# Kernel tuning notes

Measured on AMD Instinct MI355X. Metric: run time of the kernel, lower is better.

Reference implementation:

```python
import jax, jax.numpy as jnp
import numpy as np

DIM = 320
D_STATE = 32
D_CONV = 4
EXPAND = 2
HEADDIM = 80
D_INNER = EXPAND * DIM          # 640
NHEADS = D_INNER // HEADDIM     # 8
NGROUPS = 1
CONV_DIM = D_INNER + 2 * NGROUPS * D_STATE          # 704
D_IN_PROJ = 2 * D_INNER + 2 * NGROUPS * D_STATE + NHEADS  # 1352
PATCH = (16, 16, 16)
NUM_PT_EMB = 2


def setup_inputs() -> dict:
    key = jax.random.key(0)
    ks = jax.random.split(key, 16)
    B, Np = 4, 8
    x = jax.random.normal(ks[0], (B, DIM) + PATCH, dtype=jnp.float32)
    point_coords = jax.random.uniform(ks[1], (B, Np, 3), dtype=jnp.float32) * jnp.asarray(PATCH, jnp.float32)
    point_labels = jax.random.randint(ks[2], (B, Np), 0, 2)
    return {
        "x": x,
        "point_coords": point_coords,
        "ln_w": jnp.ones((DIM,), jnp.float32),
        "ln_b": jnp.zeros((DIM,), jnp.float32),
        "in_proj_w": jax.random.normal(ks[3], (D_IN_PROJ, DIM), jnp.float32) * 0.02,
        "conv_w": jax.random.normal(ks[4], (CONV_DIM, 1, D_CONV), jnp.float32) * 0.2,
        "conv_b": jax.random.normal(ks[5], (CONV_DIM,), jnp.float32) * 0.02,
        "dt_bias": jax.random.uniform(ks[6], (NHEADS,), jnp.float32, 0.0, 0.1),
        "A_log": jnp.log(jax.random.uniform(ks[7], (NHEADS,), jnp.float32, 1.0, 16.0)),
        "Dp": jnp.ones((NHEADS,), jnp.float32),
        "rms_w": jnp.ones((D_INNER,), jnp.float32),
        "out_proj_w": jax.random.normal(ks[8], (DIM, D_INNER), jnp.float32) * 0.02,
        "pe_gauss": jax.random.normal(ks[9], (3, DIM // 2), jnp.float32),
        "point_embed": jax.random.normal(ks[10], (NUM_PT_EMB, DIM), jnp.float32) * 0.02,
        "not_a_point": jax.random.normal(ks[11], (DIM,), jnp.float32) * 0.02,
        "point_labels": point_labels,
    }


def _forward(x, point_coords, ln_w, ln_b, in_proj_w, conv_w, conv_b, dt_bias,
             A_log, Dp, rms_w, out_proj_w, pe_gauss, point_embed, not_a_point,
             point_labels):
    B, C = x.shape[:2]
    img_dims = x.shape[2:]
    n_tokens = int(np.prod(img_dims))
    xf = x.reshape(B, C, n_tokens).transpose(0, 2, 1)  # (B, T, C)

    # ---- PointEncoder (SAM-style random Fourier positional embedding) ----
    pc = point_coords / jnp.asarray(PATCH, x.dtype)     # normalize to [0,1]
    pc = 2.0 * pc - 1.0
    pe = (2.0 * jnp.pi) * (pc @ pe_gauss)               # (B, Np, DIM/2)
    pemb = jnp.concatenate([jnp.sin(pe), jnp.cos(pe)], axis=-1)  # (B, Np, DIM)
    lbl = point_labels[..., None]
    safe = jnp.clip(point_labels, 0, NUM_PT_EMB - 1)
    pemb = jnp.where(lbl == -1, not_a_point, pemb + point_embed[safe])

    seq = jnp.concatenate([xf, pemb], axis=1)           # (B, L, C)
    L = seq.shape[1]

    # ---- LayerNorm ----
    mu = seq.mean(-1, keepdims=True)
    var = jnp.mean((seq - mu) ** 2, axis=-1, keepdims=True)
    xn = (seq - mu) * jax.lax.rsqrt(var + 1e-5) * ln_w + ln_b

    # ---- Mamba2 ----
    zxbcdt = xn @ in_proj_w.T                            # (B, L, 1352)
    z = zxbcdt[..., :D_INNER]
    xBC = zxbcdt[..., D_INNER:D_INNER + CONV_DIM]
    dt = zxbcdt[..., D_INNER + CONV_DIM:]                # (B, L, H)
    dt = jax.nn.softplus(dt + dt_bias)

    # causal depthwise conv1d over channels
    conv = jax.lax.conv_general_dilated(
        xBC.transpose(0, 2, 1), conv_w, (1,), [(D_CONV - 1, 0)],
        feature_group_count=CONV_DIM,
        dimension_numbers=("NCH", "OIH", "NCH"))
    xBC = jax.nn.silu((conv + conv_b[None, :, None]).transpose(0, 2, 1))

    xs = xBC[..., :D_INNER].reshape(B, L, NHEADS, HEADDIM)
    Bm = xBC[..., D_INNER:D_INNER + D_STATE]             # (B, L, N), ngroups=1
    Cm = xBC[..., D_INNER + D_STATE:]                    # (B, L, N)

    A = -jnp.exp(A_log)                                  # (H,)
    dA = jnp.exp(dt * A)                                 # (B, L, H)

    def step(h, inp):
        dA_t, dt_t, B_t, C_t, x_t = inp
        h = h * dA_t[:, :, None, None] + jnp.einsum('bh,bn,bhp->bhpn', dt_t, B_t, x_t)
        y = jnp.einsum('bhpn,bn->bhp', h, C_t)
        return h, y

    inps = (dA.transpose(1, 0, 2), dt.transpose(1, 0, 2),
            Bm.transpose(1, 0, 2), Cm.transpose(1, 0, 2),
            xs.transpose(1, 0, 2, 3))
    h0 = jnp.zeros((B, NHEADS, HEADDIM, D_STATE), x.dtype)
    _, ys = jax.lax.scan(step, h0, inps)                 # (L, B, H, P)
    y = ys.transpose(1, 0, 2, 3) + xs * Dp[None, None, :, None]
    y = y.reshape(B, L, D_INNER)

    # gated RMSNorm
    y = y * jax.nn.silu(z)
    y = y * jax.lax.rsqrt(jnp.mean(y * y, axis=-1, keepdims=True) + 1e-5) * rms_w
    out = y @ out_proj_w.T                               # (B, L, DIM)

    out = out[:, :n_tokens].transpose(0, 2, 1).reshape(B, C, *img_dims)
    return out


def reference(x, point_coords, ln_w, ln_b, in_proj_w, conv_w, conv_b, dt_bias,
              A_log, Dp, rms_w, out_proj_w, pe_gauss, point_embed, not_a_point,
              point_labels):
    return _forward(x, point_coords, ln_w, ln_b, in_proj_w, conv_w, conv_b,
                    dt_bias, A_log, Dp, rms_w, out_proj_w, pe_gauss,
                    point_embed, not_a_point, point_labels)
```

## Files before the change

### kernel.cpp

```cpp
#include <hip/hip_runtime.h>
#include <math.h>

#define BQ 4
#define LQ 4104
#define NTQ 4096
#define CDIM 320
#define DIP 1352
#define DI 640
#define CONVD 704
#define NH 8
#define HD 80
#define DS 32
#define MQ (BQ*LQ)
#define QC 64
#define NC 65

typedef __attribute__((ext_vector_type(8))) short bf16x8;
typedef __attribute__((ext_vector_type(4))) float f32x4;

__device__ __forceinline__ unsigned short f2bf(float f){
  union { float f; unsigned u; } v; v.f = f;
  unsigned r = v.u + 0x7FFFu + ((v.u >> 16) & 1u);
  return (unsigned short)(r >> 16);
}
__device__ __forceinline__ float bf2f(unsigned short u){
  union { unsigned u; float f; } v; v.u = ((unsigned)u) << 16;
  return v.f;
}
__device__ __forceinline__ float warp_sum(float v){
  #pragma unroll
  for (int o = 32; o; o >>= 1) v += __shfl_xor(v, o);
  return v;
}
__device__ __forceinline__ void gload16(const unsigned short* g, unsigned short* l){
  __builtin_amdgcn_global_load_lds(
      (const __attribute__((address_space(1))) unsigned int*)g,
      (__attribute__((address_space(3))) unsigned int*)l, 16, 0, 0);
}
__device__ __forceinline__ int swz64(int p, int i){
  return p*QC + (i ^ ((p & 7) << 3));
}

__global__ __launch_bounds__(256) void k_f2bf4(
    const float* __restrict__ s1, unsigned short* __restrict__ d1, int n14,
    const float* __restrict__ s2, unsigned short* __restrict__ d2, int n24)
{
  int i4 = blockIdx.x*256 + threadIdx.x;
  if (i4 < n14) {
    float4 v = ((const float4*)s1)[i4];
    unsigned short o[4] = {f2bf(v.x), f2bf(v.y), f2bf(v.z), f2bf(v.w)};
    *(uint2*)&d1[i4*4] = *(const uint2*)o;
  } else if (i4 - n14 < n24) {
    int j = i4 - n14;
    float4 v = ((const float4*)s2)[j];
    unsigned short o[4] = {f2bf(v.x), f2bf(v.y), f2bf(v.z), f2bf(v.w)};
    *(uint2*)&d2[j*4] = *(const uint2*)o;
  }
}

__global__ __launch_bounds__(256) void k_stats(
    const float* __restrict__ x, float* __restrict__ muP, float* __restrict__ s2P)
{
  int b = blockIdx.z;
  int sl = blockIdx.y;
  int cs0 = sl * 40;
  int tok = blockIdx.x*256 + threadIdx.x;
  const float* xb = x + ((size_t)b*CDIM)*NTQ;
  float s = 0.f, s2 = 0.f;
  #pragma unroll 8
  for (int c = cs0; c < cs0 + 40; c++) {
    float v = xb[(size_t)c*NTQ + tok];
    s += v; s2 = fmaf(v, v, s2);
  }
  muP[((size_t)sl*BQ + b)*NTQ + tok] = s;
  s2P[((size_t)sl*BQ + b)*NTQ + tok] = s2;
}

__global__ __launch_bounds__(256) void k_norm_t(
    const float* __restrict__ x, const float* __restrict__ muP,
    const float* __restrict__ s2P, const float* __restrict__ lnw,
    const float* __restrict__ lnb, unsigned short* __restrict__ xnh)
{
  int b = blockIdx.z;
  int c0 = blockIdx.y * 64;
  int t0 = blockIdx.x * 64;
  int t = threadIdx.x;
  int lt = t & 63, cg = t >> 6;
  const float* xb = x + ((size_t)b*CDIM)*NTQ;

  __shared__ unsigned short T[64][72];
  __shared__ float muL[64], rsL[64];
  if (t < 64) {
    float s = 0.f, s2 = 0.f;
    #pragma unroll
    for (int sl = 0; sl < 8; sl++) {
      s  += muP[((size_t)sl*BQ + b)*NTQ + t0 + t];
      s2 += s2P[((size_t)sl*BQ + b)*NTQ + t0 + t];
    }
    float mu = s*(1.0f/CDIM);
    muL[t] = mu;
    rsL[t] = rsqrtf(s2*(1.0f/CDIM) - mu*mu + 1e-5f);
  }
  __syncthreads();
  float mu = muL[lt], rs = rsL[lt];
  #pragma unroll
  for (int c = cg; c < 64; c += 4) {
    float v = xb[(size_t)(c0+c)*NTQ + t0 + lt];
    T[lt][c] = f2bf((v - mu)*rs*lnw[c0+c] + lnb[c0+c]);
  }
  __syncthreads();
  #pragma unroll
  for (int i = 0; i < 4; i++) {
    int idx = t + 256*i;
    int tok = idx >> 4, cq = idx & 15;
    *(uint2*)&xnh[((size_t)(b*LQ) + t0 + tok)*CDIM + c0 + cq*4] =
        *(const uint2*)&T[tok][cq*4];
  }
}

__global__ __launch_bounds__(320) void k_pt_ln(
    const float* __restrict__ pcoords, const float* __restrict__ lnw,
    const float* __restrict__ lnb, const float* __restrict__ pgauss,
    const float* __restrict__ pemb_w, const float* __restrict__ nap,
    const int* __restrict__ plabels, unsigned short* __restrict__ xnh)
{
  int j = blockIdx.x, b = blockIdx.y;
  int c = threadIdx.x;
  int f = (c < 160) ? c : c - 160;
  float p0 = pcoords[(b*8+j)*3+0]*(2.0f/16.0f) - 1.0f;
  float p1 = pcoords[(b*8+j)*3+1]*(2.0f/16.0f) - 1.0f;
  float p2 = pcoords[(b*8+j)*3+2]*(2.0f/16.0f) - 1.0f;
  float pe = 6.283185307179586f*(p0*pgauss[f] + p1*pgauss[160+f] + p2*pgauss[320+f]);
  float pv = (c < 160) ? sinf(pe) : cosf(pe);
  int lab = plabels[b*8+j];
  float val;
  if (lab == -1) val = nap[c];
  else {
    int safe = lab < 0 ? 0 : (lab > 1 ? 1 : lab);
    val = pv + pemb_w[safe*CDIM + c];
  }
  float s  = warp_sum(val);
  float s2 = warp_sum(val*val);
  __shared__ float r1[5], r2[5];
  int w = threadIdx.x >> 6, lane = threadIdx.x & 63;
  if (lane == 0) { r1[w] = s; r2[w] = s2; }
  __syncthreads();
  float ts = 0.f, ts2 = 0.f;
  #pragma unroll
  for (int i = 0; i < 5; i++) { ts += r1[i]; ts2 += r2[i]; }
  float mu  = ts * (1.0f/CDIM);
  float var = ts2 * (1.0f/CDIM) - mu*mu;
  float rsig = rsqrtf(var + 1e-5f);
  xnh[((size_t)b*LQ + NTQ + j)*CDIM + c] = f2bf((val - mu)*rsig*lnw[c] + lnb[c]);
}

__global__ __launch_bounds__(256) void k_gemm1_mfma(
    const unsigned short* __restrict__ Abf, const unsigned short* __restrict__ Wbf,
    unsigned short* __restrict__ zxh, float* __restrict__ dtraw)
{
  __shared__ unsigned short As[2][128*32];
  __shared__ unsigned short Bs[2][128*32];
  int id = blockIdx.x;
  int xcd = id & 7, pos = id >> 3;
  const int q = 177, r = 3;
  int swz = (xcd < r ? xcd*(q+1) : r*(q+1) + (xcd-r)*q) + pos;
  int m0 = (swz / 11) * 128;
  int n0 = (swz % 11) * 128;
  int tid = threadIdx.x;
  int lane = tid & 63, wid = tid >> 6;
  int wr = wid >> 1, wc = wid & 1;
  int fr = lane & 15, fq = lane >> 4;
  int srow = lane >> 2;
  int scol = (lane & 3) * 8;

#define G1_STAGE(buf, kk)                                                   \
  {                                                                         \
    _Pragma("unroll")                                                       \
    for (int i = 0; i < 2; i++) {                                           \
      int seg = wid + i*4;                                                  \
      int rowA = seg*16 + srow;                                             \
      int ga = m0 + rowA; if (ga > MQ-1) ga = MQ-1;                         \
      gload16(Abf + (size_t)ga*CDIM + (kk) + scol, &As[buf][seg*512]);      \
      int gb = n0 + rowA; if (gb > DIP-1) gb = DIP-1;                       \
      gload16(Wbf + (size_t)gb*CDIM + (kk) + scol, &Bs[buf][seg*512]);      \
    }                                                                       \
  }

#define G1_COMPUTE(buf)                                                     \
  {                                                                         \
    bf16x8 fa[4], fb[4];                                                    \
    _Pragma("unroll")                                                       \
    for (int i = 0; i < 4; i++) {                                           \
      fa[i] = *(const bf16x8*)&As[buf][(wr*64 + i*16 + fr)*32 + fq*8];      \
      fb[i] = *(const bf16x8*)&Bs[buf][(wc*64 + i*16 + fr)*32 + fq*8];      \
    }                                                                       \
    _Pragma("unroll")                                                       \
    for (int i = 0; i < 4; i++)                                             \
      _Pragma("unroll")                                                     \
      for (int j = 0; j < 4; j++)                                           \
        acc[i][j] = __builtin_amdgcn_mfma_f32_16x16x32_bf16(fa[i], fb[j], acc[i][j], 0, 0, 0); \
  }

  f32x4 acc[4][4] = {};
  G1_STAGE(0, 0);
  __syncthreads();
  int cur = 0;
  for (int k0 = 32; k0 < CDIM; k0 += 32) {
    G1_STAGE(cur^1, k0);
    G1_COMPUTE(cur);
    __syncthreads();
    cur ^= 1;
  }
  G1_COMPUTE(cur);

  #pragma unroll
  for (int i = 0; i < 4; i++) {
    #pragma unroll
    for (int j = 0; j < 4; j++) {
      #pragma unroll
      for (int rr = 0; rr < 4; rr++) {
        int grow = m0 + wr*64 + i*16 + fq*4 + rr;
        int gcol = n0 + wc*64 + j*16 + fr;
        if (grow < MQ && gcol < DIP) {
          float v = acc[i][j][rr];
          zxh[(size_t)grow*DIP + gcol] = f2bf(v);
          if (gcol >= DI + CONVD)
            dtraw[(size_t)grow*NH + (gcol - (DI + CONVD))] = v;
        }
      }
    }
  }
}

__global__ __launch_bounds__(256) void k_conv(
    const unsigned short* __restrict__ zxh, const float* __restrict__ cw,
    const float* __restrict__ cb, unsigned short* __restrict__ xcb)
{
  const int nC4 = CONVD/4;
  int gid = blockIdx.x*256 + threadIdx.x;
  if (gid >= (MQ/8)*nC4) return;
  int c4 = gid % nC4;
  int mb = gid / nC4;
  int m0 = mb*8;
  int l0 = m0 % LQ;
  int c0 = c4*4;
  float4 cbv = *(const float4*)(cb + c0);
  float4 w0 = *(const float4*)(cw + (c0+0)*4);
  float4 w1 = *(const float4*)(cw + (c0+1)*4);
  float4 w2 = *(const float4*)(cw + (c0+2)*4);
  float4 w3 = *(const float4*)(cw + (c0+3)*4);
  const float* wp[4] = {(const float*)&w0, (const float*)&w1,
                        (const float*)&w2, (const float*)&w3};
  float vals[11][4];
  #pragma unroll
  for (int r = 0; r < 11; r++) {
    int ls = l0 - 3 + r;
    uint2 u = make_uint2(0,0);
    if (ls >= 0)
      u = *(const uint2*)(zxh + (size_t)(m0-3+r)*DIP + DI + c0);
    vals[r][0] = bf2f((unsigned short)(u.x & 0xffff));
    vals[r][1] = bf2f((unsigned short)(u.x >> 16));
    vals[r][2] = bf2f((unsigned short)(u.y & 0xffff));
    vals[r][3] = bf2f((unsigned short)(u.y >> 16));
  }
  const float* cbp = (const float*)&cbv;
  #pragma unroll
  for (int u = 0; u < 8; u++) {
    unsigned short o[4];
    #pragma unroll
    for (int ch = 0; ch < 4; ch++) {
      float a = cbp[ch];
      #pragma unroll
      for (int j = 0; j < 4; j++)
        a = fmaf(vals[u+j][ch], wp[ch][j], a);
      o[ch] = f2bf(a / (1.f + __expf(-a)));
    }
    *(uint2*)(xcb + (size_t)(m0+u)*CONVD + c0) = *(const uint2*)o;
  }
}

__global__ __launch_bounds__(256) void k_cumsum_state(
    const float* __restrict__ dtraw, const float* __restrict__ dt_bias,
    const float* __restrict__ A_log, const unsigned short* __restrict__ xcb,
    float* __restrict__ dtb, float* __restrict__ cs, float* __restrict__ Dc,
    float* __restrict__ Sbuf)
{
  int c = blockIdx.x, h = blockIdx.y, b = blockIdx.z;
  int len = LQ - c*QC; if (len > QC) len = QC;
  int t = threadIdx.x;
  int lane = t & 63, wid = t >> 6;
  int fr = lane & 15, fq = lane >> 4;
  int m0 = b*LQ + c*QC;

  __shared__ unsigned short XT[HD*QC];
  __shared__ unsigned short BwT[DS*QC];
  __shared__ float ws[QC];

  for (int idx = t; idx < (HD/8)*QC; idx += 256) {
    int pg = idx % 10, i = idx / 10;
    uint4 v = make_uint4(0,0,0,0);
    if (i < len)
      v = *(const uint4*)(xcb + (size_t)(m0+i)*CONVD + h*HD + pg*8);
    union { uint4 u; unsigned short us[8]; } cv; cv.u = v;
    #pragma unroll
    for (int e = 0; e < 8; e++)
      XT[swz64(pg*8+e, i)] = cv.us[e];
  }

  if (t < QC) {
    float A = -expf(A_log[h]);
    float sp = 0.f;
    if (t < len) {
      float v = dtraw[((size_t)(m0+t))*NH + h] + dt_bias[h];
      sp = (v > 20.f) ? v : log1pf(expf(v));
      dtb[((size_t)(m0+t))*NH + h] = sp;
    }
    float a = sp * A;
    #pragma unroll
    for (int off = 1; off < 64; off <<= 1) {
      float pv = __shfl_up(a, off, 64);
      if (t >= off) a += pv;
    }
    cs[((size_t)(b*NH+h)*NC + c)*QC + t] = a;
    if (t == len-1) Dc[(b*NH+h)*NC + c] = expf(a);
    float aEnd = __shfl(a, len-1, 64);
    ws[t] = (t < len) ? __expf(aEnd - a) * sp : 0.f;
  }
  __syncthreads();
  for (int idx = t; idx < DS*QC; idx += 256) {
    int n = idx & 31, i = idx >> 5;
    float v = (i < len) ? bf2f(xcb[(size_t)(m0+i)*CONVD + DI + n]) * ws[i] : 0.f;
    BwT[swz64(n, i)] = f2bf(v);
  }
  __syncthreads();

  size_t base = ((size_t)(b*NC + c)*NH + h)*(HD*DS);
  for (int tp = wid; tp < 10; tp += 4) {
    int pi = tp >> 1, ni = tp & 1;
    f32x4 acc = {};
    #pragma unroll
    for (int ks = 0; ks < 2; ks++) {
      bf16x8 fa = *(const bf16x8*)&XT[swz64(pi*16 + fr, ks*32 + fq*8)];
      bf16x8 fb = *(const bf16x8*)&BwT[swz64(ni*16 + fr, ks*32 + fq*8)];
      acc = __builtin_amdgcn_mfma_f32_16x16x32_bf16(fa, fb, acc, 0, 0, 0);
    }
    #pragma unroll
    for (int rr = 0; rr < 4; rr++)
      Sbuf[base + (size_t)(pi*16 + fq*4 + rr)*DS + ni*16 + fr] = acc[rr];
  }
}

__global__ __launch_bounds__(256) void k_state_scan(
    float* __restrict__ Sbuf, const float* __restrict__ Dc,
    float* __restrict__ H0)
{
  int tid = blockIdx.x*256 + threadIdx.x;
  int pn = tid % (HD*DS);
  int bh = tid / (HD*DS);
  int b = bh >> 3, h = bh & 7;
  float hst = 0.f;
  for (int c = 0; c < NC; c++) {
    size_t idx = ((size_t)(b*NC + c)*NH + h)*(HD*DS) + pn;
    float sv = Sbuf[idx];
    H0[idx] = hst;
    hst = hst * Dc[bh*NC + c] + sv;
  }
}

__global__ __launch_bounds__(256) void k_chunk_y_mfma(
    const unsigned short* __restrict__ xcb, const unsigned short* __restrict__ zxh,
    const float* __restrict__ dtb, const float* __restrict__ cs,
    const float* __restrict__ H0, const float* __restrict__ Dp,
    unsigned short* __restrict__ ygb)
{
  int c = blockIdx.x, h = blockIdx.y, b = blockIdx.z;
  int len = LQ - c*QC; if (len > QC) len = QC;
  int t = threadIdx.x;
  int lane = t & 63, wid = t >> 6;
  int fr = lane & 15, fq = lane >> 4;
  int m0 = b*LQ + c*QC;

  __shared__ unsigned short XT[HD*QC];
  __shared__ unsigned short Wt[4*16*32];
  __shared__ float slA[QC], dtlA[QC], elA[QC];

  const float* csb = cs + ((size_t)(b*NH+h)*NC + c)*QC;

  for (int idx = t; idx < (HD/8)*QC; idx += 256) {
    int pg = idx % 10, i = idx / 10;
    uint4 v = make_uint4(0,0,0,0);
    if (i < len)
      v = *(const uint4*)(xcb + (size_t)(m0+i)*CONVD + h*HD + pg*8);
    union { uint4 u; unsigned short us[8]; } cv; cv.u = v;
    #pragma unroll
    for (int e = 0; e < 8; e++)
      XT[swz64(pg*8+e, i)] = cv.us[e];
  }
  if (t < QC) {
    float s = csb[t];
    slA[t] = s;
    elA[t] = __expf(s);
    dtlA[t] = (t < len) ? dtb[((size_t)(m0+t))*NH + h] : 0.f;
  }
  __syncthreads();

  int row16 = wid*16 + fr;
  bf16x8 fa = {};
  if (row16 < len)
    fa = *(const bf16x8*)(xcb + (size_t)(m0+row16)*CONVD + DI + DS + fq*8);

  size_t hb = ((size_t)(b*NC + c)*NH + h)*(HD*DS);
  f32x4 acc[5];
  #pragma unroll
  for (int j = 0; j < 5; j++) {
    int p = j*16 + fr;
    const float* hp = H0 + hb + (size_t)p*DS + fq*8;
    float4 ha = *(const float4*)hp;
    float4 hbv = *(const float4*)(hp + 4);
    bf16x8 fb;
    fb[0]=(short)f2bf(ha.x);  fb[1]=(short)f2bf(ha.y);
    fb[2]=(short)f2bf(ha.z);  fb[3]=(short)f2bf(ha.w);
    fb[4]=(short)f2bf(hbv.x); fb[5]=(short)f2bf(hbv.y);
    fb[6]=(short)f2bf(hbv.z); fb[7]=(short)f2bf(hbv.w);
    f32x4 z = {};
    acc[j] = __builtin_amdgcn_mfma_f32_16x16x32_bf16(fa, fb, z, 0, 0, 0);
  }
  #pragma unroll
  for (int rr = 0; rr < 4; rr++) {
    float el = elA[wid*16 + fq*4 + rr];
    #pragma unroll
    for (int j = 0; j < 5; j++) acc[j][rr] *= el;
  }

  int wbase = wid << 9;
  for (int sc = 0; sc < 2; sc++) {
    int i0 = sc*32;
    #pragma unroll
    for (int jt = 0; jt < 2; jt++) {
      int col = i0 + jt*16 + fr;
      bf16x8 fbv = {};
      if (col < len)
        fbv = *(const bf16x8*)(xcb + (size_t)(m0+col)*CONVD + DI + fq*8);
      float sc_col = slA[col], dt_col = dtlA[col];
      f32x4 z = {};
      f32x4 g = __builtin_amdgcn_mfma_f32_16x16x32_bf16(fa, fbv, z, 0, 0, 0);
      #pragma unroll
      for (int rr = 0; rr < 4; rr++) {
        int lr = fq*4 + rr;
        int row = wid*16 + lr;
        float v = 0.f;
        if (col <= row)
          v = g[rr] * __expf(slA[row] - sc_col) * dt_col;
        int lc = jt*16 + fr;
        int slot = (lc >> 3) ^ (lr & 3);
        Wt[wbase + (lr<<5) + (slot<<3) + (lc&7)] = f2bf(v);
      }
    }
    bf16x8 wa = *(const bf16x8*)&Wt[wbase + (fr<<5) + ((fq ^ (fr&3))<<3)];
    #pragma unroll
    for (int j = 0; j < 5; j++) {
      int p = j*16 + fr;
      bf16x8 xb = *(const bf16x8*)&XT[swz64(p, i0 + fq*8)];
      acc[j] = __builtin_amdgcn_mfma_f32_16x16x32_bf16(wa, xb, acc[j], 0, 0, 0);
    }
  }

  float dpv = Dp[h];
  #pragma unroll
  for (int rr = 0; rr < 4; rr++) {
    int l = wid*16 + fq*4 + rr;
    if (l >= len) continue;
    size_t m = m0 + l;
    #pragma unroll
    for (int j = 0; j < 5; j++) {
      int p = j*16 + fr;
      int cc = h*HD + p;
      float xv = bf2f(XT[swz64(p, l)]);
      float y = acc[j][rr] + xv*dpv;
      float zv = bf2f(zxh[m*DIP + cc]);
      y *= zv / (1.f + __expf(-zv));
      ygb[m*DI + cc] = f2bf(y);
    }
  }
}

__global__ __launch_bounds__(256) void k_rms_scale(
    unsigned short* __restrict__ ygb, const float* __restrict__ rsw)
{
  int t = threadIdx.x;
  int grp = t >> 5;
  int gl = t & 31;
  size_t m = (size_t)blockIdx.x*8 + grp;
  unsigned short* row = ygb + m*DI;
  float v[5][4];
  float ss = 0.f;
  #pragma unroll
  for (int k = 0; k < 5; k++) {
    uint2 u = *(const uint2*)(row + (gl + 32*k)*4);
    v[k][0] = bf2f((unsigned short)(u.x & 0xffff));
    v[k][1] = bf2f((unsigned short)(u.x >> 16));
    v[k][2] = bf2f((unsigned short)(u.y & 0xffff));
    v[k][3] = bf2f((unsigned short)(u.y >> 16));
    ss += v[k][0]*v[k][0] + v[k][1]*v[k][1] + v[k][2]*v[k][2] + v[k][3]*v[k][3];
  }
  #pragma unroll
  for (int o = 16; o; o >>= 1) ss += __shfl_xor(ss, o, 32);
  float rsv = rsqrtf(ss*(1.0f/DI) + 1e-5f);
  #pragma unroll
  for (int k = 0; k < 5; k++) {
    float4 wv = *(const float4*)(rsw + (gl + 32*k)*4);
    unsigned short o4[4];
    o4[0] = f2bf(v[k][0]*rsv*wv.x);
    o4[1] = f2bf(v[k][1]*rsv*wv.y);
    o4[2] = f2bf(v[k][2]*rsv*wv.z);
    o4[3] = f2bf(v[k][3]*rsv*wv.w);
    *(uint2*)(row + (gl + 32*k)*4) = *(const uint2*)o4;
  }
}

__global__ __launch_bounds__(256) void k_gemm2_mfma(
    const unsigned short* __restrict__ W2h, const unsigned short* __restrict__ Ygh,
    float* __restrict__ out)
{
  __shared__ unsigned short As[2][128*32];
  __shared__ unsigned short Bs[2][128*32];
  int id = blockIdx.x;
  int xcd = id & 7, pos = id >> 3;
  const int q = 48, r = 3;
  int swz = (xcd < r ? xcd*(q+1) : r*(q+1) + (xcd-r)*q) + pos;
  int c0 = (swz % 3) * 128;
  int t0 = (swz / 3) * 128;
  int tid = threadIdx.x;
  int lane = tid & 63, wid = tid >> 6;
  int wr = wid >> 1, wc = wid & 1;
  int fr = lane & 15, fq = lane >> 4;
  int srow = lane >> 2;
  int scol = (lane & 3) * 8;

#define G2_STAGE(buf, kk)                                                   \
  {                                                                         \
    _Pragma("unroll")                                                       \
    for (int i = 0; i < 2; i++) {                                           \
      int seg = wid + i*4;                                                  \
      int rowA = seg*16 + srow;                                             \
      int ga = c0 + rowA; if (ga > CDIM-1) ga = CDIM-1;                     \
      gload16(W2h + (size_t)ga*DI + (kk) + scol, &As[buf][seg*512]);        \
      int gb = t0 + rowA; if (gb > MQ-1) gb = MQ-1;                         \
      gload16(Ygh + (size_t)gb*DI + (kk) + scol, &Bs[buf][seg*512]);        \
    }                                                                       \
  }

#define G2_COMPUTE(buf)                                                     \
  {                                                                         \
    bf16x8 fa[4], fb[4];                                                    \
    _Pragma("unroll")                                                       \
    for (int i = 0; i < 4; i++) {                                           \
      fa[i] = *(const bf16x8*)&As[buf][(wr*64 + i*16 + fr)*32 + fq*8];      \
      fb[i] = *(const bf16x8*)&Bs[buf][(wc*64 + i*16 + fr)*32 + fq*8];      \
    }                                                                       \
    _Pragma("unroll")                                                       \
    for (int i = 0; i < 4; i++)                                             \
      _Pragma("unroll")                                                     \
      for (int j = 0; j < 4; j++)                                           \
        acc[i][j] = __builtin_amdgcn_mfma_f32_16x16x32_bf16(fa[i], fb[j], acc[i][j], 0, 0, 0); \
  }

  f32x4 acc[4][4] = {};
  G2_STAGE(0, 0);
  __syncthreads();
  int cur = 0;
  for (int k0 = 32; k0 < DI; k0 += 32) {
    G2_STAGE(cur^1, k0);
    G2_COMPUTE(cur);
    __syncthreads();
    cur ^= 1;
  }
  G2_COMPUTE(cur);

  #pragma unroll
  for (int i = 0; i < 4; i++) {
    #pragma unroll
    for (int j = 0; j < 4; j++) {
      #pragma unroll
      for (int rr = 0; rr < 4; rr++) {
        int ch  = c0 + wr*64 + i*16 + fq*4 + rr;
        int tok = t0 + wc*64 + j*16 + fr;
        if (ch < CDIM && tok < MQ) {
          int b = tok / LQ, l = tok % LQ;
          if (l < NTQ)
            out[((size_t)(b*CDIM + ch))*NTQ + l] = acc[i][j][rr];
        }
      }
    }
  }
}

extern "C" void kernel_launch(void* const* d_in, const int* in_sizes, int n_in,
                              void* d_out, int out_size, void* d_ws, size_t ws_size,
                              hipStream_t stream)
{
  const float* x       = (const float*)d_in[0];
  const float* pc      = (const float*)d_in[1];
  const float* lnw     = (const float*)d_in[2];
  const float* lnb     = (const float*)d_in[3];
  const float* w1      = (const float*)d_in[4];
  const float* cw      = (const float*)d_in[5];
  const float* cb      = (const float*)d_in[6];
  const float* dt_bias = (const float*)d_in[7];
  const float* A_log   = (const float*)d_in[8];
  const float* Dp      = (const float*)d_in[9];
  const float* rsw     = (const float*)d_in[10];
  const float* w2      = (const float*)d_in[11];
  const float* pg      = (const float*)d_in[12];
  const float* pew     = (const float*)d_in[13];
  const float* nap     = (const float*)d_in[14];
  const int*   plab    = (const int*)d_in[15];
  float* out = (float*)d_out;

  unsigned short* xnh  = (unsigned short*)d_ws;
  unsigned short* zxh  = xnh + (size_t)MQ*CDIM;
  float* dtraw = (float*)(zxh + (size_t)MQ*DIP);
  unsigned short* xcb  = (unsigned short*)(dtraw + (size_t)MQ*NH);
  float* dtb = (float*)(xcb + (size_t)MQ*CONVD);
  float* cs  = dtb + (size_t)MQ*NH;
  float* Dc  = cs  + (size_t)BQ*NH*NC*QC;
  float* Sb  = Dc  + (size_t)BQ*NH*NC;
  float* H0  = Sb;
  unsigned short* ygb = (unsigned short*)(Sb + (size_t)BQ*NC*NH*HD*DS);
  unsigned short* w1h = ygb + (size_t)MQ*DI;
  unsigned short* w2h = w1h + (size_t)DIP*CDIM;
  float* muP = (float*)(w2h + (size_t)CDIM*DI);
  float* s2P = muP + (size_t)8*BQ*NTQ;

  k_f2bf4<<<((DIP*CDIM + CDIM*DI)/4 + 255)/256, 256, 0, stream>>>(
      w1, w1h, DIP*CDIM/4, w2, w2h, CDIM*DI/4);
  dim3 gs(NTQ/256, 8, BQ);
  k_stats<<<gs, 256, 0, stream>>>(x, muP, s2P);
  dim3 gn(NTQ/64, CDIM/64, BQ);
  k_norm_t<<<gn, 256, 0, stream>>>(x, muP, s2P, lnw, lnb, xnh);
  dim3 gp(8, BQ);
  k_pt_ln<<<gp, 320, 0, stream>>>(pc, lnw, lnb, pg, pew, nap, plab, xnh);
  k_gemm1_mfma<<<129*11, 256, 0, stream>>>(xnh, w1h, zxh, dtraw);
  k_conv<<<((MQ/8)*(CONVD/4) + 255)/256, 256, 0, stream>>>(zxh, cw, cb, xcb);
  dim3 gc(NC, NH, BQ);
  k_cumsum_state<<<gc, 256, 0, stream>>>(dtraw, dt_bias, A_log, xcb, dtb, cs, Dc, Sb);
  k_state_scan<<<(BQ*NH*HD*DS)/256, 256, 0, stream>>>(Sb, Dc, H0);
  k_chunk_y_mfma<<<gc, 256, 0, stream>>>(xcb, zxh, dtb, cs, H0, Dp, ygb);
  k_rms_scale<<<MQ/8, 256, 0, stream>>>(ygb, rsw);
  k_gemm2_mfma<<<129*3, 256, 0, stream>>>(w2h, ygb, out);
}
```

Before: 159.4 us.

## Fold RMSNorm into out-proj epilogue, merge prep kernels, store chunk states as bf16

Removes the separate RMS-scale pass. The chunk-y kernel now emits per-head sum-of-squares partials, the rms weight is folded into the bf16 out-proj weights, and gemm2 applies the per-token rsqrt in its epilogue. The weight conversion, LayerNorm stats and point-embedding kernels are merged into one launch, and the state scan writes bf16 initial states so chunk-y loads them directly. This cuts launches and a full read-modify-write of the y buffer. In exchange it adds a small ssum8 buffer, and the RMS statistic is now taken from fp32 y before bf16 rounding.

```diff
diff --git a/kernel.cpp b/kernel.cpp
--- a/kernel.cpp
+++ b/kernel.cpp
@@ -41,39 +41,90 @@
   return p*QC + (i ^ ((p & 7) << 3));
 }
 
-__global__ __launch_bounds__(256) void k_f2bf4(
-    const float* __restrict__ s1, unsigned short* __restrict__ d1, int n14,
-    const float* __restrict__ s2, unsigned short* __restrict__ d2, int n24)
-{
-  int i4 = blockIdx.x*256 + threadIdx.x;
-  if (i4 < n14) {
-    float4 v = ((const float4*)s1)[i4];
-    unsigned short o[4] = {f2bf(v.x), f2bf(v.y), f2bf(v.z), f2bf(v.w)};
-    *(uint2*)&d1[i4*4] = *(const uint2*)o;
-  } else if (i4 - n14 < n24) {
-    int j = i4 - n14;
-    float4 v = ((const float4*)s2)[j];
-    unsigned short o[4] = {f2bf(v.x), f2bf(v.y), f2bf(v.z), f2bf(v.w)};
-    *(uint2*)&d2[j*4] = *(const uint2*)o;
-  }
-}
-
-__global__ __launch_bounds__(256) void k_stats(
-    const float* __restrict__ x, float* __restrict__ muP, float* __restrict__ s2P)
-{
-  int b = blockIdx.z;
-  int sl = blockIdx.y;
-  int cs0 = sl * 40;
-  int tok = blockIdx.x*256 + threadIdx.x;
-  const float* xb = x + ((size_t)b*CDIM)*NTQ;
-  float s = 0.f, s2 = 0.f;
-  #pragma unroll 8
-  for (int c = cs0; c < cs0 + 40; c++) {
-    float v = xb[(size_t)c*NTQ + tok];
-    s += v; s2 = fmaf(v, v, s2);
-  }
-  muP[((size_t)sl*BQ + b)*NTQ + tok] = s;
-  s2P[((size_t)sl*BQ + b)*NTQ + tok] = s2;
+__global__ __launch_bounds__(256) void k_prep(
+    const float* __restrict__ w1, unsigned short* __restrict__ w1h,
+    const float* __restrict__ w2, const float* __restrict__ rsw,
+    unsigned short* __restrict__ w2h,
+    const float* __restrict__ x, float* __restrict__ muP, float* __restrict__ s2P,
+    const float* __restrict__ pcoords, const float* __restrict__ lnw,
+    const float* __restrict__ lnb, const float* __restrict__ pgauss,
+    const float* __restrict__ pemb_w, const float* __restrict__ nap,
+    const int* __restrict__ plabels, unsigned short* __restrict__ xnh)
+{
+  const int N1 = DIP*CDIM/4;
+  const int N2 = CDIM*DI/4;
+  const int NBW = (N1 + N2 + 255)/256;
+  int bid = blockIdx.x;
+  int t = threadIdx.x;
+
+  if (bid < NBW) {
+    int i4 = bid*256 + t;
+    if (i4 < N1) {
+      float4 v = ((const float4*)w1)[i4];
+      unsigned short o[4] = {f2bf(v.x), f2bf(v.y), f2bf(v.z), f2bf(v.w)};
+      *(uint2*)&w1h[i4*4] = *(const uint2*)o;
+    } else if (i4 - N1 < N2) {
+      int j = i4 - N1;
+      float4 v = ((const float4*)w2)[j];
+      float4 wv = *(const float4*)(rsw + (j*4) % DI);
+      unsigned short o[4] = {f2bf(v.x*wv.x), f2bf(v.y*wv.y),
+                             f2bf(v.z*wv.z), f2bf(v.w*wv.w)};
+      *(uint2*)&w2h[j*4] = *(const uint2*)o;
+    }
+    return;
+  }
+  bid -= NBW;
+  if (bid < 512) {
+    int xblk = bid & 15, sl = (bid >> 4) & 7, b = bid >> 7;
+    int cs0 = sl * 40;
+    int tok = xblk*256 + t;
+    const float* xb = x + ((size_t)b*CDIM)*NTQ;
+    float s = 0.f, s2 = 0.f;
+    #pragma unroll 8
+    for (int c = cs0; c < cs0 + 40; c++) {
+      float v = xb[(size_t)c*NTQ + tok];
+      s += v; s2 = fmaf(v, v, s2);
+    }
+    muP[((size_t)sl*BQ + b)*NTQ + tok] = s;
+    s2P[((size_t)sl*BQ + b)*NTQ + tok] = s2;
+    return;
+  }
+  bid -= 512;
+  int j = bid & 7, b = bid >> 3;
+  float p0 = pcoords[(b*8+j)*3+0]*(2.0f/16.0f) - 1.0f;
+  float p1 = pcoords[(b*8+j)*3+1]*(2.0f/16.0f) - 1.0f;
+  float p2 = pcoords[(b*8+j)*3+2]*(2.0f/16.0f) - 1.0f;
+  int lab = plabels[b*8+j];
+  int safe = lab < 0 ? 0 : (lab > 1 ? 1 : lab);
+  float vA, vB = 0.f;
+  {
+    int cc = t;
+    int f = (cc < 160) ? cc : cc - 160;
+    float pe = 6.283185307179586f*(p0*pgauss[f] + p1*pgauss[160+f] + p2*pgauss[320+f]);
+    float pv = (cc < 160) ? sinf(pe) : cosf(pe);
+    vA = (lab == -1) ? nap[cc] : pv + pemb_w[safe*CDIM + cc];
+  }
+  if (t < 64) {
+    int cc = t + 256;
+    int f = cc - 160;
+    float pe = 6.283185307179586f*(p0*pgauss[f] + p1*pgauss[160+f] + p2*pgauss[320+f]);
+    float pv = cosf(pe);
+    vB = (lab == -1) ? nap[cc] : pv + pemb_w[safe*CDIM + cc];
+  }
+  float s  = warp_sum(vA + vB);
+  float s2 = warp_sum(vA*vA + vB*vB);
+  __shared__ float r1[4], r2[4];
+  int w = t >> 6, lane = t & 63;
+  if (lane == 0) { r1[w] = s; r2[w] = s2; }
+  __syncthreads();
+  float ts  = r1[0]+r1[1]+r1[2]+r1[3];
+  float ts2 = r2[0]+r2[1]+r2[2]+r2[3];
+  float mu   = ts * (1.0f/CDIM);
+  float rsig = rsqrtf(ts2*(1.0f/CDIM) - mu*mu + 1e-5f);
+  size_t base = ((size_t)b*LQ + NTQ + j)*CDIM;
+  xnh[base + t] = f2bf((vA - mu)*rsig*lnw[t] + lnb[t]);
+  if (t < 64)
+    xnh[base + t + 256] = f2bf((vB - mu)*rsig*lnw[t+256] + lnb[t+256]);
 }
 
 __global__ __launch_bounds__(256) void k_norm_t(
@@ -116,42 +167,6 @@
     *(uint2*)&xnh[((size_t)(b*LQ) + t0 + tok)*CDIM + c0 + cq*4] =
         *(const uint2*)&T[tok][cq*4];
   }
-}
-
-__global__ __launch_bounds__(320) void k_pt_ln(
-    const float* __restrict__ pcoords, const float* __restrict__ lnw,
-    const float* __restrict__ lnb, const float* __restrict__ pgauss,
-    const float* __restrict__ pemb_w, const float* __restrict__ nap,
-    const int* __restrict__ plabels, unsigned short* __restrict__ xnh)
-{
-  int j = blockIdx.x, b = blockIdx.y;
-  int c = threadIdx.x;
-  int f = (c < 160) ? c : c - 160;
-  float p0 = pcoords[(b*8+j)*3+0]*(2.0f/16.0f) - 1.0f;
-  float p1 = pcoords[(b*8+j)*3+1]*(2.0f/16.0f) - 1.0f;
-  float p2 = pcoords[(b*8+j)*3+2]*(2.0f/16.0f) - 1.0f;
-  float pe = 6.283185307179586f*(p0*pgauss[f] + p1*pgauss[160+f] + p2*pgauss[320+f]);
-  float pv = (c < 160) ? sinf(pe) : cosf(pe);
-  int lab = plabels[b*8+j];
-  float val;
-  if (lab == -1) val = nap[c];
-  else {
-    int safe = lab < 0 ? 0 : (lab > 1 ? 1 : lab);
-    val = pv + pemb_w[safe*CDIM + c];
-  }
-  float s  = warp_sum(val);
-  float s2 = warp_sum(val*val);
-  __shared__ float r1[5], r2[5];
-  int w = threadIdx.x >> 6, lane = threadIdx.x & 63;
-  if (lane == 0) { r1[w] = s; r2[w] = s2; }
-  __syncthreads();
-  float ts = 0.f, ts2 = 0.f;
-  #pragma unroll
-  for (int i = 0; i < 5; i++) { ts += r1[i]; ts2 += r2[i]; }
-  float mu  = ts * (1.0f/CDIM);
-  float var = ts2 * (1.0f/CDIM) - mu*mu;
-  float rsig = rsqrtf(var + 1e-5f);
-  xnh[((size_t)b*LQ + NTQ + j)*CDIM + c] = f2bf((val - mu)*rsig*lnw[c] + lnb[c]);
 }
 
 __global__ __launch_bounds__(256) void k_gemm1_mfma(
@@ -351,8 +366,8 @@
 }
 
 __global__ __launch_bounds__(256) void k_state_scan(
-    float* __restrict__ Sbuf, const float* __restrict__ Dc,
-    float* __restrict__ H0)
+    const float* __restrict__ Sbuf, const float* __restrict__ Dc,
+    unsigned short* __restrict__ H0h)
 {
   int tid = blockIdx.x*256 + threadIdx.x;
   int pn = tid % (HD*DS);
@@ -362,7 +377,7 @@
   for (int c = 0; c < NC; c++) {
     size_t idx = ((size_t)(b*NC + c)*NH + h)*(HD*DS) + pn;
     float sv = Sbuf[idx];
-    H0[idx] = hst;
+    H0h[idx] = f2bf(hst);
     hst = hst * Dc[bh*NC + c] + sv;
   }
 }
@@ -370,8 +385,8 @@
 __global__ __launch_bounds__(256) void k_chunk_y_mfma(
     const unsigned short* __restrict__ xcb, const unsigned short* __restrict__ zxh,
     const float* __restrict__ dtb, const float* __restrict__ cs,
-    const float* __restrict__ H0, const float* __restrict__ Dp,
-    unsigned short* __restrict__ ygb)
+    const unsigned short* __restrict__ H0h, const float* __restrict__ Dp,
+    unsigned short* __restrict__ ygb, float* __restrict__ ssum8)
 {
   int c = blockIdx.x, h = blockIdx.y, b = blockIdx.z;
   int len = LQ - c*QC; if (len > QC) len = QC;
@@ -414,14 +429,7 @@
   #pragma unroll
   for (int j = 0; j < 5; j++) {
     int p = j*16 + fr;
-    const float* hp = H0 + hb + (size_t)p*DS + fq*8;
-    float4 ha = *(const float4*)hp;
-    float4 hbv = *(const float4*)(hp + 4);
-    bf16x8 fb;
-    fb[0]=(short)f2bf(ha.x);  fb[1]=(short)f2bf(ha.y);
-    fb[2]=(short)f2bf(ha.z);  fb[3]=(short)f2bf(ha.w);
-    fb[4]=(short)f2bf(hbv.x); fb[5]=(short)f2bf(hbv.y);
-    fb[6]=(short)f2bf(hbv.z); fb[7]=(short)f2bf(hbv.w);
+    bf16x8 fb = *(const bf16x8*)(H0h + hb + (size_t)p*DS + fq*8);
     f32x4 z = {};
     acc[j] = __builtin_amdgcn_mfma_f32_16x16x32_bf16(fa, fb, z, 0, 0, 0);
   }
@@ -471,6 +479,7 @@
     int l = wid*16 + fq*4 + rr;
     if (l >= len) continue;
     size_t m = m0 + l;
+    float ssp = 0.f;
     #pragma unroll
     for (int j = 0; j < 5; j++) {
       int p = j*16 + fr;
@@ -480,47 +489,17 @@
       float zv = bf2f(zxh[m*DIP + cc]);
       y *= zv / (1.f + __expf(-zv));
       ygb[m*DI + cc] = f2bf(y);
-    }
-  }
-}
-
-__global__ __launch_bounds__(256) void k_rms_scale(
-    unsigned short* __restrict__ ygb, const float* __restrict__ rsw)
-{
-  int t = threadIdx.x;
-  int grp = t >> 5;
-  int gl = t & 31;
-  size_t m = (size_t)blockIdx.x*8 + grp;
-  unsigned short* row = ygb + m*DI;
-  float v[5][4];
-  float ss = 0.f;
-  #pragma unroll
-  for (int k = 0; k < 5; k++) {
-    uint2 u = *(const uint2*)(row + (gl + 32*k)*4);
-    v[k][0] = bf2f((unsigned short)(u.x & 0xffff));
-    v[k][1] = bf2f((unsigned short)(u.x >> 16));
-    v[k][2] = bf2f((unsigned short)(u.y & 0xffff));
-    v[k][3] = bf2f((unsigned short)(u.y >> 16));
-    ss += v[k][0]*v[k][0] + v[k][1]*v[k][1] + v[k][2]*v[k][2] + v[k][3]*v[k][3];
-  }
-  #pragma unroll
-  for (int o = 16; o; o >>= 1) ss += __shfl_xor(ss, o, 32);
-  float rsv = rsqrtf(ss*(1.0f/DI) + 1e-5f);
-  #pragma unroll
-  for (int k = 0; k < 5; k++) {
-    float4 wv = *(const float4*)(rsw + (gl + 32*k)*4);
-    unsigned short o4[4];
-    o4[0] = f2bf(v[k][0]*rsv*wv.x);
-    o4[1] = f2bf(v[k][1]*rsv*wv.y);
-    o4[2] = f2bf(v[k][2]*rsv*wv.z);
-    o4[3] = f2bf(v[k][3]*rsv*wv.w);
-    *(uint2*)(row + (gl + 32*k)*4) = *(const uint2*)o4;
+      ssp = fmaf(y, y, ssp);
+    }
+    #pragma unroll
+    for (int o = 1; o < 16; o <<= 1) ssp += __shfl_xor(ssp, o);
+    if (fr == 0) ssum8[m*NH + h] = ssp;
   }
 }
 
 __global__ __launch_bounds__(256) void k_gemm2_mfma(
     const unsigned short* __restrict__ W2h, const unsigned short* __restrict__ Ygh,
-    float* __restrict__ out)
+    const float* __restrict__ ssum8, float* __restrict__ out)
 {
   __shared__ unsigned short As[2][128*32];
   __shared__ unsigned short Bs[2][128*32];
@@ -577,6 +556,19 @@
   }
   G2_COMPUTE(cur);
 
+  float rsvj[4];
+  #pragma unroll
+  for (int j = 0; j < 4; j++) {
+    int tok = t0 + wc*64 + j*16 + fr;
+    float ss = 0.f;
+    if (tok < MQ) {
+      float4 a = *(const float4*)(ssum8 + (size_t)tok*NH);
+      float4 bb = *(const float4*)(ssum8 + (size_t)tok*NH + 4);
+      ss = (a.x + a.y + a.z + a.w) + (bb.x + bb.y + bb.z + bb.w);
+    }
+    rsvj[j] = rsqrtf(ss*(1.0f/DI) + 1e-5f);
+  }
+
   #pragma unroll
   for (int i = 0; i < 4; i++) {
     #pragma unroll
@@ -588,7 +580,7 @@
         if (ch < CDIM && tok < MQ) {
           int b = tok / LQ, l = tok % LQ;
           if (l < NTQ)
-            out[((size_t)(b*CDIM + ch))*NTQ + l] = acc[i][j][rr];
+            out[((size_t)(b*CDIM + ch))*NTQ + l] = acc[i][j][rr] * rsvj[j];
         }
       }
     }
@@ -625,27 +617,25 @@
   float* cs  = dtb + (size_t)MQ*NH;
   float* Dc  = cs  + (size_t)BQ*NH*NC*QC;
   float* Sb  = Dc  + (size_t)BQ*NH*NC;
-  float* H0  = Sb;
-  unsigned short* ygb = (unsigned short*)(Sb + (size_t)BQ*NC*NH*HD*DS);
+  unsigned short* H0h = (unsigned short*)(Sb + (size_t)BQ*NC*NH*HD*DS);
+  unsigned short* ygb = H0h + (size_t)BQ*NC*NH*HD*DS;
   unsigned short* w1h = ygb + (size_t)MQ*DI;
   unsigned short* w2h = w1h + (size_t)DIP*CDIM;
   float* muP = (float*)(w2h + (size_t)CDIM*DI);
   float* s2P = muP + (size_t)8*BQ*NTQ;
-
-  k_f2bf4<<<((DIP*CDIM + CDIM*DI)/4 + 255)/256, 256, 0, stream>>>(
-      w1, w1h, DIP*CDIM/4, w2, w2h, CDIM*DI/4);
-  dim3 gs(NTQ/256, 8, BQ);
-  k_stats<<<gs, 256, 0, stream>>>(x, muP, s2P);
+  float* ssum8 = s2P + (size_t)8*BQ*NTQ;
+
+  const int NBW = (DIP*CDIM/4 + CDIM*DI/4 + 255)/256;
+  k_prep<<<NBW + 512 + 32, 256, 0, stream>>>(
+      w1, w1h, w2, rsw, w2h, x, muP, s2P,
+      pc, lnw, lnb, pg, pew, nap, plab, xnh);
   dim3 gn(NTQ/64, CDIM/64, BQ);
   k_norm_t<<<gn, 256, 0, stream>>>(x, muP, s2P, lnw, lnb, xnh);
-  dim3 gp(8, BQ);
-  k_pt_ln<<<gp, 320, 0, stream>>>(pc, lnw, lnb, pg, pew, nap, plab, xnh);
   k_gemm1_mfma<<<129*11, 256, 0, stream>>>(xnh, w1h, zxh, dtraw);
   k_conv<<<((MQ/8)*(CONVD/4) + 255)/256, 256, 0, stream>>>(zxh, cw, cb, xcb);
   dim3 gc(NC, NH, BQ);
   k_cumsum_state<<<gc, 256, 0, stream>>>(dtraw, dt_bias, A_log, xcb, dtb, cs, Dc, Sb);
-  k_state_scan<<<(BQ*NH*HD*DS)/256, 256, 0, stream>>>(Sb, Dc, H0);
-  k_chunk_y_mfma<<<gc, 256, 0, stream>>>(xcb, zxh, dtb, cs, H0, Dp, ygb);
-  k_rms_scale<<<MQ/8, 256, 0, stream>>>(ygb, rsw);
-  k_gemm2_mfma<<<129*3, 256, 0, stream>>>(w2h, ygb, out);
-}
+  k_state_scan<<<(BQ*NH*HD*DS)/256, 256, 0, stream>>>(Sb, Dc, H0h);
+  k_chunk_y_mfma<<<gc, 256, 0, stream>>>(xcb, zxh, dtb, cs, H0h, Dp, ygb, ssum8);
+  k_gemm2_mfma<<<129*3, 256, 0, stream>>>(w2h, ygb, ssum8, out);
+}
```

Result: faster. 149.7 us (-6.1%).
